# Performance work log

Measured on AMD Instinct MI355X. Metric: run time of the kernel, lower is better.

The kernel has to match this reference:

```python
import jax, jax.numpy as jnp
import numpy as np

N_NODES = 100000
N_EDGES = 3200000
IN_DIM = 256
HID = 16
OUT = 10


def setup_inputs() -> dict:
    key = jax.random.key(0)
    k1, k2, k3, k4, k5, k6 = jax.random.split(key, 6)
    x = jax.random.normal(k1, (N_NODES, IN_DIM), dtype=jnp.float32)
    edge_index = jax.random.randint(k2, (2, N_EDGES), 0, N_NODES, dtype=jnp.int64)
    # Glorot-style init for GCN weights, zeros for bias (PyG defaults)
    W1 = jax.random.normal(k3, (IN_DIM, HID), dtype=jnp.float32) * (1.0 / np.sqrt(IN_DIM))
    b1 = jnp.zeros((HID,), dtype=jnp.float32)
    W2 = jax.random.normal(k4, (HID, OUT), dtype=jnp.float32) * (1.0 / np.sqrt(HID))
    b2 = jnp.zeros((OUT,), dtype=jnp.float32)
    return {"x": x, "edge_index": edge_index, "W1": W1, "b1": b1, "W2": W2, "b2": b2}


def _gcn_conv(h, src, dst, W, b, num_nodes):
    # GCNConv(normalize=False): out_i = sum_{(j->i) in E} (h_j W) + b
    m = h @ W                                   # [N, F_out] small GEMM
    agg = jax.ops.segment_sum(m[src], dst, num_segments=num_nodes)  # gather+scatter-add
    return agg + b


def reference(x, edge_index, W1, b1, W2, b2):
    src = edge_index[0]  # message source (flow: source_to_target)
    dst = edge_index[1]
    n = x.shape[0]
    h = jax.nn.relu(_gcn_conv(x, src, dst, W1, b1, n))
    # F.dropout with module in eval mode -> identity
    out = _gcn_conv(h, src, dst, W2, b2, n)
    return out
```

## Files before the change

### kernel.cpp

```cpp
#include <hip/hip_runtime.h>
#include <hip/hip_bf16.h>
#include <stdint.h>

#define IN_DIM 256
#define HID 16
#define OUTD 10
#define BKT_SHIFT 8
#define BKT_W 256
#define PART_CH 8192
#define EPT 16
#define G_HIST 512
#define SSRC_CAP 8704

typedef short v8s __attribute__((ext_vector_type(8)));
typedef float v4f __attribute__((ext_vector_type(4)));

__device__ __forceinline__ float bf2f(unsigned short u) {
    return __uint_as_float(((unsigned int)u) << 16);
}
__device__ __forceinline__ unsigned short f2bf(float f) {
    unsigned int u = __float_as_uint(f);
    unsigned int lsb = (u >> 16) & 1u;
    u += 0x7fffu + lsb;
    return (unsigned short)(u >> 16);
}

__device__ __forceinline__ void split2(float f0, float f1,
                                       unsigned int& hi2, unsigned int& lo2) {
    unsigned int u0 = __float_as_uint(f0);
    unsigned int u1 = __float_as_uint(f1);
    hi2 = __builtin_amdgcn_perm(u1, u0, 0x07060302u);
    float h0 = __uint_as_float(u0 & 0xFFFF0000u);
    float h1 = __uint_as_float(u1 & 0xFFFF0000u);
    unsigned int l0 = __float_as_uint(f0 - h0);
    unsigned int l1 = __float_as_uint(f1 - h1);
    lo2 = __builtin_amdgcn_perm(l1, l0, 0x07060302u);
}

__device__ __forceinline__ int load_dst(const void* ei, int n_edges, int e, int is64) {
    return is64 ? (int)((const long long*)ei)[(size_t)n_edges + e]
                : ((const int*)ei)[(size_t)n_edges + e];
}
__device__ __forceinline__ int load_src(const void* ei, int n_edges, int e, int is64) {
    return is64 ? (int)((const long long*)ei)[e] : ((const int*)ei)[e];
}

__global__ void zero_kernel(int* __restrict__ bucket_cnt, int K) {
    for (int i = threadIdx.x; i < K; i += blockDim.x) bucket_cnt[i] = 0;
}

__global__ void setup_bhist_kernel(const void* __restrict__ x,
                                   const void* __restrict__ W1,
                                   const void* __restrict__ ei,
                                   int n_nodes, int n_edges,
                                   int* __restrict__ flags,
                                   int* __restrict__ bucket_cnt, int K,
                                   unsigned short* __restrict__ W1split) {
    __shared__ int lh[512];
    __shared__ int sflag;
    int b = blockIdx.x, t = threadIdx.x;

    if (b < 16) {
        if (t == 0) sflag = 0;
        __syncthreads();
        {
            float vw = bf2f(((const unsigned short*)W1)[t]);
            if (!(vw > -1e4f && vw < 1e4f)) sflag = 1;
        }
        __syncthreads();
        const int wf32 = sflag;
        int i = b * 256 + t;
        float w = wf32 ? ((const float*)W1)[i]
                       : bf2f(((const unsigned short*)W1)[i]);
        unsigned short hi = f2bf(w);
        unsigned short lo = f2bf(w - bf2f(hi));
        int k = i >> 4, n = i & 15;
        int kk = k >> 5, qd = (k >> 3) & 3, j = k & 7;
        int idx = ((kk * 4 + qd) * 16 + n) * 8 + j;
        W1split[idx] = hi;
        W1split[4096 + idx] = lo;
        return;
    }
    if (b == 16) {
        if (t < 64) {
            const unsigned short* xs = (const unsigned short*)x;
            const unsigned short* ws = (const unsigned short*)W1;
            bool badx = false, badw = false;
#pragma unroll
            for (int q = 0; q < 4; ++q) {
                float vx = bf2f(xs[t + 64 * q]);
                float vw = bf2f(ws[t + 64 * q]);
                if (!(vx > -1e4f && vx < 1e4f)) badx = true;
                if (!(vw > -1e4f && vw < 1e4f)) badw = true;
            }
            const unsigned long long* e64 = (const unsigned long long*)ei;
            bool big = false;
#pragma unroll
            for (int q = 0; q < 2; ++q)
                if (e64[t + 64 * q] >= (unsigned long long)n_nodes) big = true;
            int xf32 = __any(badx) ? 1 : 0;
            int wf32 = __any(badw) ? 1 : 0;
            int is64 = __any(big) ? 0 : 1;
            if (t == 0) { flags[0] = is64; flags[1] = xf32; flags[2] = wf32; }
        }
        return;
    }

    if (t == 0) sflag = 1;
    __syncthreads();
    {
        const unsigned long long* e64 = (const unsigned long long*)ei;
        if (t < 128 && e64[t] >= (unsigned long long)n_nodes) sflag = 0;
    }
    __syncthreads();
    const int is64 = sflag;
    for (int i = t; i < 512; i += 256) lh[i] = 0;
    __syncthreads();
    int vbid = b - 17;
    int stride = G_HIST * 256;
    for (int e = vbid * 256 + t; e < n_edges; e += stride) {
        int d = load_dst(ei, n_edges, e, is64);
        atomicAdd(&lh[d >> BKT_SHIFT], 1);
    }
    __syncthreads();
    for (int i = t; i < K; i += 256)
        if (lh[i]) atomicAdd(&bucket_cnt[i], lh[i]);
}

__global__ void bscan_kernel(const int* __restrict__ bucket_cnt, int K,
                             int* __restrict__ bucket_off, int* __restrict__ bcur,
                             int* __restrict__ row_off, int n_nodes, int n_edges) {
    __shared__ int ts[256];
    int t = threadIdx.x;
    const int KP = (K + 255) / 256;
    int base = t * KP;
    int local[8];
    int s = 0;
    for (int q = 0; q < KP; ++q) {
        int idx = base + q;
        int v = (idx < K) ? bucket_cnt[idx] : 0;
        local[q] = v; s += v;
    }
    ts[t] = s;
    __syncthreads();
    for (int off = 1; off < 256; off <<= 1) {
        int v = (t >= off) ? ts[t - off] : 0;
        __syncthreads();
        ts[t] += v;
        __syncthreads();
    }
    int ex = ts[t] - s;
    for (int q = 0; q < KP; ++q) {
        int idx = base + q;
        if (idx < K) { bucket_off[idx] = ex; bcur[idx] = ex; }
        ex += local[q];
    }
    if (t == 255) bucket_off[K] = ex;
    if (t == 0) row_off[n_nodes] = n_edges;
}

__global__ __launch_bounds__(512, 4) void part_gemm1_kernel(
        const void* __restrict__ ei, int n_edges,
        int* __restrict__ bcur, unsigned int* __restrict__ pairs,
        const void* __restrict__ xp_,
        const unsigned short* __restrict__ W1split,
        unsigned short* __restrict__ m1, int n_nodes,
        const int* __restrict__ flags, int K, int g_part) {
    __shared__ int lh[512];
    __shared__ int gdelta[512];
    __shared__ unsigned int spairs[PART_CH];
    __shared__ unsigned short sbkt[PART_CH];
    int t = threadIdx.x;

    if ((int)blockIdx.x < g_part) {
        int begin = blockIdx.x * PART_CH;
        int is64 = flags[0];
        lh[t] = 0;

        int dloc[EPT];
#pragma unroll
        for (int i = 0; i < EPT; ++i) {
            int e = begin + i * 512 + t;
            dloc[i] = (e < n_edges) ? load_dst(ei, n_edges, e, is64) : -1;
        }
        __syncthreads();
#pragma unroll
        for (int i = 0; i < EPT; ++i)
            if (dloc[i] >= 0) atomicAdd(&lh[dloc[i] >> BKT_SHIFT], 1);
        __syncthreads();

        int c = lh[t];
        for (int off = 1; off < 512; off <<= 1) {
            int add = (t >= off) ? lh[t - off] : 0;
            __syncthreads();
            lh[t] += add;
            __syncthreads();
        }
        int ex = lh[t] - c;
        if (c > 0) gdelta[t] = atomicAdd(&bcur[t], c) - ex;
        lh[t] = ex;
        __syncthreads();

#pragma unroll
        for (int i = 0; i < EPT; ++i) {
            int e = begin + i * 512 + t;
            if (dloc[i] >= 0) {
                int srcv = load_src(ei, n_edges, e, is64);
                int bb = dloc[i] >> BKT_SHIFT;
                int lpos = atomicAdd(&lh[bb], 1);
                spairs[lpos] = ((unsigned)srcv << 8) | ((unsigned)dloc[i] & (BKT_W - 1));
                sbkt[lpos] = (unsigned short)bb;
            }
        }
        __syncthreads();

        int total = n_edges - begin; if (total > PART_CH) total = PART_CH;
        for (int j = t; j < total; j += 512)
            pairs[gdelta[sbkt[j]] + j] = spairs[j];
        return;
    }

    const int xf32 = flags[1];
    int vb = blockIdx.x - g_part;
    int g_gemm = gridDim.x - g_part;
    int lane = t & 63;
    int wave = t >> 6;
    int col  = lane & 15;
    int quad = lane >> 4;
    int n_tiles = (n_nodes + 15) >> 4;
    const unsigned short* Whi = W1split;
    const unsigned short* Wlo = W1split + 4096;

    if (!xf32) {
        const unsigned short* x = (const unsigned short*)xp_;
        for (int tile = vb * 8 + wave; tile < n_tiles; tile += g_gemm * 8) {
            int row = tile * 16 + col;
            int r = row < n_nodes ? row : n_nodes - 1;
            const unsigned short* xp = x + (size_t)r * IN_DIM + quad * 8;
            v8s a[8];
#pragma unroll
            for (int kk = 0; kk < 8; ++kk)
                a[kk] = *(const v8s*)(xp + kk * 32);
            v4f acc1 = {0.f, 0.f, 0.f, 0.f};
            v4f acc2 = {0.f, 0.f, 0.f, 0.f};
#pragma unroll
            for (int kk = 0; kk < 8; ++kk) {
                v8s bh = *(const v8s*)&Whi[(kk * 64 + lane) * 8];
                v8s bl = *(const v8s*)&Wlo[(kk * 64 + lane) * 8];
                acc1 = __builtin_amdgcn_mfma_f32_16x16x32_bf16(a[kk], bh, acc1, 0, 0, 0);
                acc2 = __builtin_amdgcn_mfma_f32_16x16x32_bf16(a[kk], bl, acc2, 0, 0, 0);
            }
#pragma unroll
            for (int rg = 0; rg < 4; ++rg) {
                int node = tile * 16 + quad * 4 + rg;
                if (node < n_nodes)
                    m1[(size_t)node * HID + col] = f2bf(acc1[rg] + acc2[rg]);
            }
        }
    } else {
        const float* x = (const float*)xp_;
        for (int tile = vb * 8 + wave; tile < n_tiles; tile += g_gemm * 8) {
            int row = tile * 16 + col;
            int r = row < n_nodes ? row : n_nodes - 1;
            const float* xp = x + (size_t)r * IN_DIM + quad * 8;
            float4 u[16];
#pragma unroll
            for (int kk = 0; kk < 8; ++kk) {
                u[2 * kk]     = *(const float4*)(xp + kk * 32);
                u[2 * kk + 1] = *(const float4*)(xp + kk * 32 + 4);
            }
            v4f acc1 = {0.f, 0.f, 0.f, 0.f};
            v4f acc2 = {0.f, 0.f, 0.f, 0.f};
#pragma unroll
            for (int kk = 0; kk < 8; ++kk) {
                union { unsigned int w[4]; v8s v; } ahi, alo;
#pragma unroll
                for (int pj = 0; pj < 2; ++pj) {
                    float4 ff = u[2 * kk + pj];
                    split2(ff.x, ff.y, ahi.w[2 * pj],     alo.w[2 * pj]);
                    split2(ff.z, ff.w, ahi.w[2 * pj + 1], alo.w[2 * pj + 1]);
                }
                v8s bh = *(const v8s*)&Whi[(kk * 64 + lane) * 8];
                v8s bl = *(const v8s*)&Wlo[(kk * 64 + lane) * 8];
                acc1 = __builtin_amdgcn_mfma_f32_16x16x32_bf16(ahi.v, bh, acc1, 0, 0, 0);
                acc2 = __builtin_amdgcn_mfma_f32_16x16x32_bf16(ahi.v, bl, acc2, 0, 0, 0);
                acc2 = __builtin_amdgcn_mfma_f32_16x16x32_bf16(alo.v, bh, acc2, 0, 0, 0);
            }
#pragma unroll
            for (int rg = 0; rg < 4; ++rg) {
                int node = tile * 16 + quad * 4 + rg;
                if (node < n_nodes)
                    m1[(size_t)node * HID + col] = f2bf(acc1[rg] + acc2[rg]);
            }
        }
    }
}

__global__ __launch_bounds__(1024) void csr_agg1_kernel(
        const unsigned int* __restrict__ pairs,
        const int* __restrict__ bucket_off,
        const unsigned short* __restrict__ m1,
        const void* __restrict__ b1p,
        int* __restrict__ row_off, int* __restrict__ csr_src,
        unsigned short* __restrict__ h,
        int n_nodes, const int* __restrict__ flags) {
    __shared__ unsigned int ssrc[SSRC_CAP];
    __shared__ int deg[BKT_W];
    __shared__ int cur[BKT_W];
    __shared__ int ts[BKT_W];
    int blk = blockIdx.x;
    int nbase = blk << BKT_SHIFT;
    int NL = n_nodes - nbase; if (NL > BKT_W) NL = BKT_W;
    int beg = bucket_off[blk], end = bucket_off[blk + 1];
    int t = threadIdx.x;

    if (t < BKT_W) deg[t] = 0;
    __syncthreads();
    for (int k = beg + t; k < end; k += 1024)
        atomicAdd(&deg[pairs[k] & (BKT_W - 1)], 1);
    __syncthreads();
    if (t < BKT_W) ts[t] = deg[t];
    __syncthreads();
    for (int off = 1; off < BKT_W; off <<= 1) {
        int v = 0;
        if (t < BKT_W && t >= off) v = ts[t - off];
        __syncthreads();
        if (t < BKT_W) ts[t] += v;
        __syncthreads();
    }
    if (t < BKT_W) {
        int exl = ts[t] - deg[t];
        cur[t] = exl;
        if (t < NL) row_off[nbase + t] = beg + exl;
    }
    __syncthreads();
    for (int k = beg + t; k < end; k += 1024) {
        unsigned int pr = pairs[k];
        int dl = pr & (BKT_W - 1);
        int pos = atomicAdd(&cur[dl], 1);
        int src = (int)(pr >> 8);
        csr_src[beg + pos] = src;
        if (pos < SSRC_CAP) ssrc[pos] = (unsigned)src;
    }
    __syncthreads();

    const int wf32 = flags[2];
    int q = t & 3, grp = t >> 2;
    float b0, b1v, b2v, b3;
    if (wf32) {
        const float* b = (const float*)b1p + q * 4;
        b0 = b[0]; b1v = b[1]; b2v = b[2]; b3 = b[3];
    } else {
        const unsigned short* b = (const unsigned short*)b1p + q * 4;
        b0 = bf2f(b[0]); b1v = bf2f(b[1]); b2v = bf2f(b[2]); b3 = bf2f(b[3]);
    }
    for (int nl = grp; nl < NL; nl += 256) {
        int sL = ts[nl] - deg[nl];
        int eL = ts[nl];
        float a0 = 0.f, a1 = 0.f, a2 = 0.f, a3 = 0.f;
        int k = sL;
        for (; k + 8 <= eL; k += 8) {
            int sidx[8];
            uint2 v[8];
#pragma unroll
            for (int u = 0; u < 8; ++u)
                sidx[u] = (k + u < SSRC_CAP) ? (int)ssrc[k + u]
                                             : csr_src[beg + k + u];
#pragma unroll
            for (int u = 0; u < 8; ++u)
                v[u] = *(const uint2*)(m1 + (size_t)sidx[u] * HID + q * 4);
#pragma unroll
            for (int u = 0; u < 8; ++u) {
                a0 += bf2f((unsigned short)(v[u].x));
                a1 += bf2f((unsigned short)(v[u].x >> 16));
                a2 += bf2f((unsigned short)(v[u].y));
                a3 += bf2f((unsigned short)(v[u].y >> 16));
            }
        }
        for (; k < eL; ++k) {
            int s = (k < SSRC_CAP) ? (int)ssrc[k] : csr_src[beg + k];
            uint2 v = *(const uint2*)(m1 + (size_t)s * HID + q * 4);
            a0 += bf2f((unsigned short)(v.x));
            a1 += bf2f((unsigned short)(v.x >> 16));
            a2 += bf2f((unsigned short)(v.y));
            a3 += bf2f((unsigned short)(v.y >> 16));
        }
        float r0 = fmaxf(a0 + b0, 0.f);
        float r1 = fmaxf(a1 + b1v, 0.f);
        float r2 = fmaxf(a2 + b2v, 0.f);
        float r3 = fmaxf(a3 + b3, 0.f);
        uint2 packed;
        packed.x = (unsigned int)f2bf(r0) | ((unsigned int)f2bf(r1) << 16);
        packed.y = (unsigned int)f2bf(r2) | ((unsigned int)f2bf(r3) << 16);
        *(uint2*)(h + (size_t)(nbase + nl) * HID + q * 4) = packed;
    }
}

__device__ __forceinline__ v4f gather_bf16(const unsigned short* __restrict__ src,
                                           const int* __restrict__ csr_src,
                                           int beg, int end, int q) {
    float a0 = 0.f, a1 = 0.f, a2 = 0.f, a3 = 0.f;
    int k = beg;
    for (; k + 16 <= end; k += 16) {
        uint2 v[16];
#pragma unroll
        for (int u = 0; u < 16; ++u) {
            int s = csr_src[k + u];
            v[u] = *(const uint2*)(src + (size_t)s * HID + q * 4);
        }
#pragma unroll
        for (int u = 0; u < 16; ++u) {
            a0 += bf2f((unsigned short)(v[u].x));
            a1 += bf2f((unsigned short)(v[u].x >> 16));
            a2 += bf2f((unsigned short)(v[u].y));
            a3 += bf2f((unsigned short)(v[u].y >> 16));
        }
    }
    for (; k + 4 <= end; k += 4) {
        uint2 v[4];
#pragma unroll
        for (int u = 0; u < 4; ++u) {
            int s = csr_src[k + u];
            v[u] = *(const uint2*)(src + (size_t)s * HID + q * 4);
        }
#pragma unroll
        for (int u = 0; u < 4; ++u) {
            a0 += bf2f((unsigned short)(v[u].x));
            a1 += bf2f((unsigned short)(v[u].x >> 16));
            a2 += bf2f((unsigned short)(v[u].y));
            a3 += bf2f((unsigned short)(v[u].y >> 16));
        }
    }
    for (; k < end; ++k) {
        int s = csr_src[k];
        uint2 v = *(const uint2*)(src + (size_t)s * HID + q * 4);
        a0 += bf2f((unsigned short)(v.x));
        a1 += bf2f((unsigned short)(v.x >> 16));
        a2 += bf2f((unsigned short)(v.y));
        a3 += bf2f((unsigned short)(v.y >> 16));
    }
    v4f r = {a0, a1, a2, a3};
    return r;
}

__global__ void agg2_out_kernel(const unsigned short* __restrict__ h,
                                const int* __restrict__ row_off,
                                const int* __restrict__ csr_src,
                                const void* __restrict__ W2p,
                                const void* __restrict__ b2p,
                                void* __restrict__ out, int n_nodes,
                                const int* __restrict__ flags) {
    __shared__ float Ws[HID * OUTD];
    __shared__ float bs[OUTD];
    const int xf32 = flags[1], wf32 = flags[2];
    if (threadIdx.x < HID * OUTD)
        Ws[threadIdx.x] = wf32 ? ((const float*)W2p)[threadIdx.x]
                               : bf2f(((const unsigned short*)W2p)[threadIdx.x]);
    if (threadIdx.x < OUTD)
        bs[threadIdx.x] = wf32 ? ((const float*)b2p)[threadIdx.x]
                               : bf2f(((const unsigned short*)b2p)[threadIdx.x]);
    __syncthreads();

    int t = blockIdx.x * blockDim.x + threadIdx.x;
    int node = t >> 2;
    if (node >= n_nodes) return;
    int q = t & 3;
    v4f a = gather_bf16(h, csr_src, row_off[node], row_off[node + 1], q);

    float o[OUTD];
#pragma unroll
    for (int od = 0; od < OUTD; ++od) {
        float s = 0.f;
#pragma unroll
        for (int j = 0; j < 4; ++j)
            s = fmaf(a[j], Ws[(q * 4 + j) * OUTD + od], s);
        o[od] = s;
    }
#pragma unroll
    for (int od = 0; od < OUTD; ++od) {
        o[od] += __shfl_xor(o[od], 1);
        o[od] += __shfl_xor(o[od], 2);
        o[od] += bs[od];
    }

    if (xf32) {
        float2* po = (float2*)((float*)out + (size_t)node * OUTD);
        if (q == 0) {
            po[0] = make_float2(o[0], o[1]);
            po[1] = make_float2(o[2], o[3]);
        } else if (q == 1) {
            po[2] = make_float2(o[4], o[5]);
            po[3] = make_float2(o[6], o[7]);
        } else if (q == 2) {
            po[4] = make_float2(o[8], o[9]);
        }
    } else {
        unsigned int* po = (unsigned int*)((unsigned short*)out + (size_t)node * OUTD);
        if (q == 0) {
            po[0] = (unsigned int)f2bf(o[0]) | ((unsigned int)f2bf(o[1]) << 16);
            po[1] = (unsigned int)f2bf(o[2]) | ((unsigned int)f2bf(o[3]) << 16);
        } else if (q == 1) {
            po[2] = (unsigned int)f2bf(o[4]) | ((unsigned int)f2bf(o[5]) << 16);
            po[3] = (unsigned int)f2bf(o[6]) | ((unsigned int)f2bf(o[7]) << 16);
        } else if (q == 2) {
            po[4] = (unsigned int)f2bf(o[8]) | ((unsigned int)f2bf(o[9]) << 16);
        }
    }
}

__global__ void sentinel_kernel(float* __restrict__ out) {
    if (blockIdx.x == 0 && threadIdx.x < 16) out[threadIdx.x] = 123456.0f;
}

extern "C" void kernel_launch(void* const* d_in, const int* in_sizes, int n_in,
                              void* d_out, int out_size, void* d_ws, size_t ws_size,
                              hipStream_t stream) {
    const void* x  = d_in[0];
    const void* ei = d_in[1];
    const void* W1 = d_in[2];
    const void* b1 = d_in[3];
    const void* W2 = d_in[4];
    const void* b2 = d_in[5];

    const int n_nodes = in_sizes[0] / IN_DIM;
    const int n_edges = in_sizes[1] / 2;
    const int K = (n_nodes + BKT_W - 1) / BKT_W;

    char* p = (char*)d_ws;
    auto align = [](size_t v) { return (v + 255) & ~(size_t)255; };
    size_t off = 0;
    int* flags      = (int*)(p + off); off = align(off + 256);
    unsigned short* w1split = (unsigned short*)(p + off); off = align(off + 8192 * 2);
    int* bucket_cnt = (int*)(p + off); off = align(off + (size_t)K * 4);
    int* bucket_off = (int*)(p + off); off = align(off + ((size_t)K + 1) * 4);
    int* bcur       = (int*)(p + off); off = align(off + (size_t)K * 4);
    int* row_off    = (int*)(p + off); off = align(off + ((size_t)n_nodes + 1) * 4);
    int* csr_src    = (int*)(p + off); off = align(off + (size_t)n_edges * 4);
    unsigned int* pairs = (unsigned int*)(p + off); off = align(off + (size_t)n_edges * 4);
    unsigned short* m1 = (unsigned short*)(p + off); off = align(off + (size_t)n_nodes * HID * 2);
    unsigned short* h  = (unsigned short*)(p + off); off = align(off + (size_t)n_nodes * HID * 2);

    if (ws_size < off) {
        sentinel_kernel<<<1, 64, 0, stream>>>((float*)d_out);
        return;
    }

    const int n_tiles16 = (n_nodes + 15) >> 4;
    const int g_gemm = (n_tiles16 + 7) / 8;
    const int g_part = (n_edges + PART_CH - 1) / PART_CH;

    zero_kernel<<<1, 256, 0, stream>>>(bucket_cnt, K);

    setup_bhist_kernel<<<17 + G_HIST, 256, 0, stream>>>(
        x, W1, ei, n_nodes, n_edges, flags, bucket_cnt, K, w1split);

    bscan_kernel<<<1, 256, 0, stream>>>(bucket_cnt, K, bucket_off, bcur,
                                        row_off, n_nodes, n_edges);

    part_gemm1_kernel<<<g_part + g_gemm, 512, 0, stream>>>(
        ei, n_edges, bcur, pairs, x, w1split, m1, n_nodes, flags, K, g_part);

    csr_agg1_kernel<<<K, 1024, 0, stream>>>(pairs, bucket_off, m1, b1,
                                            row_off, csr_src, h, n_nodes, flags);

    {
        long long threads = (long long)n_nodes * 4;
        agg2_out_kernel<<<(int)((threads + 255) / 256), 256, 0, stream>>>(
            h, row_off, csr_src, W2, b2, d_out, n_nodes, flags);
    }
}
```

Before: 289.9 us.

## Prefetch x into cache during histogram; drop sbkt via binary search

Adds extra blocks to the setup/histogram kernel that stream the whole x buffer (bf16-sized range) so it is resident in the large last-level cache before the GEMM reads it, with a dummy flag write to keep the loads alive. The partition kernel also drops the per-edge bucket shared array and recovers each element's bucket by binary search over the exclusive-scan offsets, which cuts LDS use and may raise occupancy at the cost of extra LDS reads per element. The prefetch adds memory traffic that competes with the histogram pass. Note that lh holds running end positions after the scatter, so the search semantics must match those offsets.

```diff
diff --git a/kernel.cpp b/kernel.cpp
--- a/kernel.cpp
+++ b/kernel.cpp
@@ -10,6 +10,7 @@
 #define PART_CH 8192
 #define EPT 16
 #define G_HIST 512
+#define G_PREF 512
 #define SSRC_CAP 8704
 
 typedef short v8s __attribute__((ext_vector_type(8)));
@@ -52,7 +53,7 @@
 __global__ void setup_bhist_kernel(const void* __restrict__ x,
                                    const void* __restrict__ W1,
                                    const void* __restrict__ ei,
-                                   int n_nodes, int n_edges,
+                                   int n_nodes, int n_edges, int x_bytes,
                                    int* __restrict__ flags,
                                    int* __restrict__ bucket_cnt, int K,
                                    unsigned short* __restrict__ W1split) {
@@ -103,6 +104,18 @@
             int is64 = __any(big) ? 0 : 1;
             if (t == 0) { flags[0] = is64; flags[1] = xf32; flags[2] = wf32; }
         }
+        return;
+    }
+    if (b >= 17 + G_HIST) {
+        const float4* x4 = (const float4*)x;
+        int n4 = x_bytes >> 4;
+        int vb = b - 17 - G_HIST;
+        float acc = 0.f;
+        for (int i = vb * 256 + t; i < n4; i += G_PREF * 256) {
+            float4 v = x4[i];
+            acc += v.x + v.y + v.z + v.w;
+        }
+        if (__float_as_uint(acc) == 0xDEADBEEFu) flags[32] = 1;
         return;
     }
 
@@ -169,7 +182,6 @@
     __shared__ int lh[512];
     __shared__ int gdelta[512];
     __shared__ unsigned int spairs[PART_CH];
-    __shared__ unsigned short sbkt[PART_CH];
     int t = threadIdx.x;
 
     if ((int)blockIdx.x < g_part) {
@@ -209,14 +221,19 @@
                 int bb = dloc[i] >> BKT_SHIFT;
                 int lpos = atomicAdd(&lh[bb], 1);
                 spairs[lpos] = ((unsigned)srcv << 8) | ((unsigned)dloc[i] & (BKT_W - 1));
-                sbkt[lpos] = (unsigned short)bb;
             }
         }
         __syncthreads();
 
         int total = n_edges - begin; if (total > PART_CH) total = PART_CH;
-        for (int j = t; j < total; j += 512)
-            pairs[gdelta[sbkt[j]] + j] = spairs[j];
+        for (int j = t; j < total; j += 512) {
+            unsigned int pv = spairs[j];
+            int bb = 0;
+#pragma unroll
+            for (int s = 256; s > 0; s >>= 1)
+                if (lh[bb + s - 1] <= j) bb += s;
+            pairs[gdelta[bb] + j] = pv;
+        }
         return;
     }
 
@@ -525,6 +542,9 @@
     const int n_nodes = in_sizes[0] / IN_DIM;
     const int n_edges = in_sizes[1] / 2;
     const int K = (n_nodes + BKT_W - 1) / BKT_W;
+    const int x_bytes = in_sizes[0];
+
+    const int pref_bytes = n_nodes * IN_DIM * 2;
 
     char* p = (char*)d_ws;
     auto align = [](size_t v) { return (v + 255) & ~(size_t)255; };
@@ -551,8 +571,8 @@
 
     zero_kernel<<<1, 256, 0, stream>>>(bucket_cnt, K);
 
-    setup_bhist_kernel<<<17 + G_HIST, 256, 0, stream>>>(
-        x, W1, ei, n_nodes, n_edges, flags, bucket_cnt, K, w1split);
+    setup_bhist_kernel<<<17 + G_HIST + G_PREF, 256, 0, stream>>>(
+        x, W1, ei, n_nodes, n_edges, pref_bytes, flags, bucket_cnt, K, w1split);
 
     bscan_kernel<<<1, 256, 0, stream>>>(bucket_cnt, K, bucket_off, bcur,
                                         row_off, n_nodes, n_edges);
```

Measured after the change: 289.0 us. Within noise of the previous version (-0.3%).
